# Kernel optimization log

Hardware: AMD Instinct MI355X
Metric: run time of the kernel (lower is better)

Reference implementation:

```python
import jax, jax.numpy as jnp
import numpy as np

B, L, C = 4, 4096, 2048
NH, K = 32, 16
F = C // NH  # head_dim = 64
LR = 1.0     # config.inner_net_lr
EPS = 1e-6


def setup_inputs() -> dict:
    key = jax.random.key(0)
    ks = jax.random.split(key, 8)
    s = 0.02
    return {
        "hidden_states": jax.random.normal(ks[0], (B, L, C), jnp.float32),
        "q_w": jax.random.normal(ks[1], (C, C), jnp.float32) * s,
        "k_w": jax.random.normal(ks[2], (C, C), jnp.float32) * s,
        "v_w": jax.random.normal(ks[3], (C, C), jnp.float32) * s,
        "o_w": jax.random.normal(ks[4], (C, C), jnp.float32) * s,
        "lin_w": jax.random.normal(ks[5], (NH, 1, C), jnp.float32) * s,
        "lin_b": jnp.zeros((NH, 1), jnp.float32),
        "ln_w": jnp.ones((NH, F), jnp.float32),
        "ln_b": jnp.zeros((NH, F), jnp.float32),
        "W1": jax.random.normal(ks[6], (NH, F, F), jnp.float32) * s,
        "b1": jnp.zeros((NH, 1, F), jnp.float32),
    }


def _ln(z, g, b):
    # LayerNormFunction.forward over last dim (head_dim)
    mu = z.mean(-1, keepdims=True)
    var = jnp.mean((z - mu) ** 2, axis=-1, keepdims=True)
    x_hat = (z - mu) * jax.lax.rsqrt(var + EPS)
    return g * x_hat + b


def _ln_l2_bwd(z, target, g, b):
    # decoder_ln_bwd: grad of 0.5*||LN(z) - target||^2 w.r.t. z, fused LN fwd+bwd
    mu = z.mean(-1, keepdims=True)
    var = jnp.mean((z - mu) ** 2, axis=-1, keepdims=True)
    std = jnp.sqrt(var + EPS)
    x_hat = (z - mu) / std
    gy = (g * x_hat + b - target) * g  # grad_x_hat
    return (F * gy - gy.sum(-1, keepdims=True)
            - x_hat * (gy * x_hat).sum(-1, keepdims=True)) / (F * std)


def reference(hidden_states, q_w, k_w, v_w, o_w, lin_w, lin_b, ln_w, ln_b, W1, b1):
    nc = L // K  # number of inner chunks

    def proj(w):
        x = hidden_states @ w.T                      # [B,L,C]
        x = x.reshape(B, nc, K, NH, F)
        return jnp.moveaxis(x, 3, 1)                 # [B,NH,nc,K,F]

    XC, XB, XA = proj(q_w), proj(k_w), proj(v_w)

    # per-head ilr gate: vmap(F.linear) over heads, softplus activation
    Xr = hidden_states.reshape(B, nc, K, C)
    ilr = jax.nn.softplus(jnp.einsum('bnkc,hoc->bhnko', Xr, lin_w)
                          + lin_b[None, :, None, None, :])   # [B,NH,nc,K,1]
    token_idx = 1.0 / jnp.arange(1, K + 1, dtype=jnp.float32)
    coeff = (LR * token_idx)[None, None, None, :, None] * ilr / F  # [B,NH,nc,K,1]

    gamma = ln_w[None, :, None, :]  # [1,NH,1,F]
    beta = ln_b[None, :, None, :]
    mask = jnp.tril(jnp.ones((K, K), jnp.float32))

    W1_0 = jnp.broadcast_to(W1[None], (B, NH, F, F))
    b1_0 = jnp.broadcast_to(b1[None], (B, NH, 1, F))

    def step(carry, xs):
        W1s, b1s = carry
        xa, xb, xc, co = xs                 # [B,NH,K,F], co: [B,NH,K,1]
        Z1 = xb @ W1s + b1s                 # inner-net forward
        gZ = _ln_l2_bwd(Z1, xa - xb, gamma, beta)  # grad_l_wrt_Z1
        Attn1 = (xc @ jnp.swapaxes(xb, -1, -2)) * mask      # tril(XC XB^T) [B,NH,K,K]
        b1_bar = b1s - (co * mask) @ gZ                      # [B,NH,K,F]
        Z1_bar = xc @ W1s - (co * Attn1) @ gZ + b1_bar       # dual-form output
        co_last = co[:, :, -1:, :]                           # [B,NH,1,1]
        W1_new = W1s - jnp.swapaxes(co_last * xb, -1, -2) @ gZ
        b1_new = b1_bar[:, :, -1:, :]
        xcw = xc + _ln(Z1_bar, gamma, beta)
        return (W1_new, b1_new), xcw

    xs = tuple(jnp.moveaxis(t, 2, 0) for t in (XA, XB, XC, coeff))
    _, out = jax.lax.scan(step, (W1_0, b1_0), xs)   # out: [nc,B,NH,K,F]
    out = jnp.moveaxis(out, 0, 1)                    # [B,nc,NH,K,F]
    out = jnp.swapaxes(out, 2, 3).reshape(B, L, C)   # [B,L,C]
    return out @ o_w.T
```

## Files before the change

kernel.cpp:

```cpp
#include <hip/hip_runtime.h>
#include <hip/hip_bf16.h>

#define B_ 4
#define L_ 4096
#define C_ 2048
#define NH_ 32
#define K_ 16
#define F_ 64
#define NC_ 256
#define EPS_ 1e-6f

typedef _Float16 half8 __attribute__((ext_vector_type(8)));
typedef _Float16 half4 __attribute__((ext_vector_type(4)));
typedef float f32x4 __attribute__((ext_vector_type(4)));

__device__ __forceinline__ float red16(float v) {
  int x;
  x = __builtin_amdgcn_update_dpp(0, __builtin_bit_cast(int, v), 0xB1, 0xF, 0xF, true);
  v += __builtin_bit_cast(float, x);
  x = __builtin_amdgcn_update_dpp(0, __builtin_bit_cast(int, v), 0x4E, 0xF, 0xF, true);
  v += __builtin_bit_cast(float, x);
  x = __builtin_amdgcn_update_dpp(0, __builtin_bit_cast(int, v), 0x124, 0xF, 0xF, true);
  v += __builtin_bit_cast(float, x);
  x = __builtin_amdgcn_update_dpp(0, __builtin_bit_cast(int, v), 0x128, 0xF, 0xF, true);
  v += __builtin_bit_cast(float, x);
  return v;
}

__device__ __forceinline__ void gl_lds16(const _Float16* g, _Float16* l) {
  __builtin_amdgcn_global_load_lds(
      (const __attribute__((address_space(1))) void*)g,
      (__attribute__((address_space(3))) void*)l, 16, 0, 0);
}

__global__ __launch_bounds__(256) void cast_f16(const float* __restrict__ in,
                                                _Float16* __restrict__ out, int n8) {
  int i = blockIdx.x * 256 + threadIdx.x;
  if (i >= n8) return;
  const float4* ip = (const float4*)in;
  float4 a = ip[2*i], b = ip[2*i+1];
  half8 o;
  o[0]=(_Float16)a.x; o[1]=(_Float16)a.y; o[2]=(_Float16)a.z; o[3]=(_Float16)a.w;
  o[4]=(_Float16)b.x; o[5]=(_Float16)b.y; o[6]=(_Float16)b.z; o[7]=(_Float16)b.w;
  ((half8*)out)[i] = o;
}

#define BM3 256
#define BN3 256
#define BK3 64

template<typename OT>
__global__ __launch_bounds__(512, 2) void gemm_f16_v3(
    const _Float16* __restrict__ A, const _Float16* __restrict__ Bm,
    OT* __restrict__ C0, OT* __restrict__ C1, OT* __restrict__ C2, int Kd)
{
  __shared__ __align__(16) _Float16 As[2][2][128*64];
  __shared__ __align__(16) _Float16 Bs[2][2][128*64];
  const int t = threadIdx.x;
  const int lane = t & 63;
  const int w = t >> 6;
  const int wr = w >> 2, wc = w & 3;
  const int bn = blockIdx.x, bm = blockIdx.y;
  const int ln = lane & 15, q = lane >> 4;

  const int srow = t >> 3, sc = t & 7;
  const int clg = sc ^ (2 * ((srow >> 2) & 1));

  auto stageA = [&](int kt, int h, int db) {
    const _Float16* g = A + ((long)(bm*BM3 + h*128 + srow))*Kd + (long)kt*BK3 + clg*8;
    gl_lds16(g,          &As[db][h][(size_t)srow*64 + sc*8]);
    gl_lds16(g + 64*Kd,  &As[db][h][(size_t)(64+srow)*64 + sc*8]);
  };
  auto stageB = [&](int kt, int h, int db) {
    const _Float16* g = Bm + ((long)(bn*BN3 + h*128 + srow))*Kd + (long)kt*BK3 + clg*8;
    gl_lds16(g,          &Bs[db][h][(size_t)srow*64 + sc*8]);
    gl_lds16(g + 64*Kd,  &Bs[db][h][(size_t)(64+srow)*64 + sc*8]);
  };

  f32x4 acc[8][4];
#pragma unroll
  for (int i = 0; i < 8; ++i)
#pragma unroll
    for (int j = 0; j < 4; ++j) acc[i][j] = (f32x4){0.f,0.f,0.f,0.f};

  half8 af[8][2], bf[4][2];

  stageA(0, 0, 0); stageA(0, 1, 0); stageB(0, 0, 0); stageB(0, 1, 0);

  const int NT = Kd / BK3;
  for (int kt = 0; kt < NT; ++kt) {
    const int db = kt & 1;
    const bool more = (kt + 1 < NT);
    if (more) { stageA(kt+1, 0, db^1); stageB(kt+1, 0, db^1); }
    __builtin_amdgcn_sched_barrier(0);
    if (more) asm volatile("s_waitcnt vmcnt(4)" ::: "memory");
    else      asm volatile("s_waitcnt vmcnt(0)" ::: "memory");
    __builtin_amdgcn_sched_barrier(0);
    __builtin_amdgcn_s_barrier();
    __builtin_amdgcn_sched_barrier(0);

    const _Float16* ap = &As[db][wr][0];
    const _Float16* bp = &Bs[db][wc >> 1][0];
    const int lcb = (wc & 1) * 64;

#pragma unroll
    for (int mi = 0; mi < 4; ++mi)
#pragma unroll
      for (int ks = 0; ks < 2; ++ks) {
        int lr = mi*16 + ln;
        int cp = (ks*4 + q) ^ (2*((lr>>2)&1));
        af[mi][ks] = *(const half8*)(ap + (size_t)lr*64 + cp*8);
      }
#pragma unroll
    for (int ni = 0; ni < 2; ++ni)
#pragma unroll
      for (int ks = 0; ks < 2; ++ks) {
        int lc = lcb + ni*16 + ln;
        int cp = (ks*4 + q) ^ (2*((lc>>2)&1));
        bf[ni][ks] = *(const half8*)(bp + (size_t)lc*64 + cp*8);
      }
    __builtin_amdgcn_s_setprio(1);
#pragma unroll
    for (int mi = 0; mi < 4; ++mi)
#pragma unroll
      for (int ni = 0; ni < 2; ++ni)
#pragma unroll
        for (int ks = 0; ks < 2; ++ks)
          acc[mi][ni] = __builtin_amdgcn_mfma_f32_16x16x32_f16(af[mi][ks], bf[ni][ks], acc[mi][ni], 0, 0, 0);
    __builtin_amdgcn_s_setprio(0);
    if (more) stageA(kt+1, 1, db^1);

#pragma unroll
    for (int mi = 4; mi < 8; ++mi)
#pragma unroll
      for (int ks = 0; ks < 2; ++ks) {
        int lr = mi*16 + ln;
        int cp = (ks*4 + q) ^ (2*((lr>>2)&1));
        af[mi][ks] = *(const half8*)(ap + (size_t)lr*64 + cp*8);
      }
    __builtin_amdgcn_s_setprio(1);
#pragma unroll
    for (int mi = 4; mi < 8; ++mi)
#pragma unroll
      for (int ni = 0; ni < 2; ++ni)
#pragma unroll
        for (int ks = 0; ks < 2; ++ks)
          acc[mi][ni] = __builtin_amdgcn_mfma_f32_16x16x32_f16(af[mi][ks], bf[ni][ks], acc[mi][ni], 0, 0, 0);
    __builtin_amdgcn_s_setprio(0);
    if (more) stageB(kt+1, 1, db^1);

#pragma unroll
    for (int ni = 2; ni < 4; ++ni)
#pragma unroll
      for (int ks = 0; ks < 2; ++ks) {
        int lc = lcb + ni*16 + ln;
        int cp = (ks*4 + q) ^ (2*((lc>>2)&1));
        bf[ni][ks] = *(const half8*)(bp + (size_t)lc*64 + cp*8);
      }
    __builtin_amdgcn_s_setprio(1);
#pragma unroll
    for (int mi = 4; mi < 8; ++mi)
#pragma unroll
      for (int ni = 2; ni < 4; ++ni)
#pragma unroll
        for (int ks = 0; ks < 2; ++ks)
          acc[mi][ni] = __builtin_amdgcn_mfma_f32_16x16x32_f16(af[mi][ks], bf[ni][ks], acc[mi][ni], 0, 0, 0);
    __builtin_amdgcn_s_setprio(0);

    __builtin_amdgcn_s_setprio(1);
#pragma unroll
    for (int mi = 0; mi < 4; ++mi)
#pragma unroll
      for (int ni = 2; ni < 4; ++ni)
#pragma unroll
        for (int ks = 0; ks < 2; ++ks)
          acc[mi][ni] = __builtin_amdgcn_mfma_f32_16x16x32_f16(af[mi][ks], bf[ni][ks], acc[mi][ni], 0, 0, 0);
    __builtin_amdgcn_s_setprio(0);

    __builtin_amdgcn_sched_barrier(0);
    __builtin_amdgcn_s_barrier();
    __builtin_amdgcn_sched_barrier(0);
  }

  const int reg = bn >> 3, bnl = bn & 7;
  OT* C = (reg == 0) ? C0 : ((reg == 1) ? C1 : C2);
  const int cr = q * 4;
#pragma unroll
  for (int mi = 0; mi < 8; ++mi)
#pragma unroll
    for (int ni = 0; ni < 4; ++ni)
#pragma unroll
      for (int r = 0; r < 4; ++r) {
        long row = (long)bm*BM3 + wr*128 + mi*16 + cr + r;
        long col = (long)bnl*256 + wc*64 + ni*16 + ln;
        C[row*2048L + col] = (OT)acc[mi][ni][r];
      }
}

__global__ __launch_bounds__(256) void ilr_kernel(
    const float* __restrict__ hid, const float* __restrict__ lin_w,
    const float* __restrict__ lin_b, float* __restrict__ coeff)
{
  const int t = threadIdx.x;
  const int lane = t & 63;
  const int w = t >> 6;
  const int row0 = blockIdx.x * 16 + w * 4;

  float4 hv[4][8];
#pragma unroll
  for (int r = 0; r < 4; ++r) {
    const float* hp = hid + (size_t)(row0 + r) * C_;
#pragma unroll
    for (int i = 0; i < 8; ++i) hv[r][i] = *(const float4*)(hp + i*256 + lane*4);
  }
  float res[4] = {0.f,0.f,0.f,0.f};
  for (int h = 0; h < NH_; ++h) {
    const float* wp = lin_w + (size_t)h * C_;
    float s[4] = {0.f,0.f,0.f,0.f};
#pragma unroll
    for (int i = 0; i < 8; ++i) {
      float4 wv = *(const float4*)(wp + i*256 + lane*4);
#pragma unroll
      for (int r = 0; r < 4; ++r)
        s[r] += hv[r][i].x*wv.x + hv[r][i].y*wv.y + hv[r][i].z*wv.z + hv[r][i].w*wv.w;
    }
#pragma unroll
    for (int o = 32; o > 0; o >>= 1)
#pragma unroll
      for (int r = 0; r < 4; ++r) s[r] += __shfl_xor(s[r], o, 64);
    if (lane == h) { res[0]=s[0]; res[1]=s[1]; res[2]=s[2]; res[3]=s[3]; }
  }
  if (lane < NH_) {
    float lb = lin_b[lane];
#pragma unroll
    for (int r = 0; r < 4; ++r) {
      int row = row0 + r;
      int b = row >> 12;
      int li = row & (L_ - 1);
      int k = li & (K_ - 1);
      float x = res[r] + lb;
      float sp = (x > 20.f) ? x : log1pf(expf(x));
      float v = (1.0f / (float)(k + 1)) * sp * (1.0f / (float)F_);
      coeff[((size_t)(b * NH_ + lane)) * L_ + li] = v;
    }
  }
}

struct Ck2 {
  half4 xbA[4], xsA[4];
  float co4[4], co15;
};

__device__ __forceinline__ void load_ck2(
    Ck2& c, const _Float16* Kp, const _Float16* S, const float* co,
    size_t rowbase, int hoff, size_t cobase, int n, int q, int ln)
{
#pragma unroll
  for (int kt = 0; kt < 4; ++kt) {
    size_t idx = (rowbase + ln) * C_ + hoff + 16*kt + 4*q;
    c.xbA[kt] = *(const half4*)(Kp + idx);
    c.xsA[kt] = *(const half4*)(S  + idx);
  }
#pragma unroll
  for (int r = 0; r < 4; ++r) c.co4[r] = co[cobase + (size_t)n*K_ + 4*q + r];
  c.co15 = co[cobase + (size_t)n*K_ + 15];
}

__global__ __launch_bounds__(128, 1) void scan_kernel(
    const _Float16* __restrict__ Q, const _Float16* __restrict__ Kp,
    const _Float16* __restrict__ V,
    const float* __restrict__ coeff, const float* __restrict__ W1g, const float* __restrict__ b1g,
    const float* __restrict__ ln_w, const float* __restrict__ ln_b,
    _Float16* __restrict__ OF)
{
  const int bh = blockIdx.x;
  const int b = bh >> 5, h = bh & 31;
  const int tid = threadIdx.x;
  const int lane = tid & 63;
  const bool isP = tid < 64;
  const int q = lane >> 4, ln = lane & 15;
  const int hoff = h * F_;
  const size_t cobase = (size_t)bh * L_;
  const size_t brow = (size_t)b * L_;

  __shared__ half4 gzs[4][4][64];

  half4 W1f[4][4];
#pragma unroll
  for (int kt = 0; kt < 4; ++kt)
#pragma unroll
    for (int t = 0; t < 4; ++t) {
      half4 hv;
#pragma unroll
      for (int j = 0; j < 4; ++j)
        hv[j] = (_Float16)W1g[(size_t)h*F_*F_ + (size_t)(16*kt + 4*q + j)*F_ + 16*t + ln];
      W1f[kt][t] = hv;
    }
  float b1r[4], gamt[4], bett[4];
#pragma unroll
  for (int t = 0; t < 4; ++t) {
    b1r[t]  = b1g[hoff + 16*t + ln];
    gamt[t] = ln_w[hoff + 16*t + ln];
    bett[t] = ln_b[hoff + 16*t + ln];
  }
  half4 maskA, maskI;
#pragma unroll
  for (int j = 0; j < 4; ++j) {
    maskA[j] = (_Float16)((4*q + j <= ln) ? 1.f : 0.f);
    maskI[j] = (_Float16)((4*q + j == ln) ? 1.f : 0.f);
  }
  const f32x4 zf4 = (f32x4){0.f, 0.f, 0.f, 0.f};

  const _Float16* S = isP ? V : Q;

  auto iter = [&](int i, Ck2& cur, Ck2& nxt) {
    half4 gzf[4];
    half4 xbTp[4];
    float co15p = 0.f;

    if (isP) {
      if (i < NC_) {
        co15p = cur.co15;
        if (i + 1 < NC_)
          load_ck2(nxt, Kp, S, coeff, brow + (size_t)(i+1)*K_, hoff, cobase, i+1, q, ln);
        f32x4 tgD[4];
#pragma unroll
        for (int t = 0; t < 4; ++t) {
          half4 dd = cur.xsA[t] - cur.xbA[t];
          tgD[t] = __builtin_amdgcn_mfma_f32_16x16x16f16(dd, maskI, zf4, 0, 0, 0);
          f32x4 x = __builtin_amdgcn_mfma_f32_16x16x16f16(cur.xbA[t], maskI, zf4, 0, 0, 0);
          half4 v;
#pragma unroll
          for (int r = 0; r < 4; ++r) v[r] = (_Float16)x[r];
          xbTp[t] = v;
        }
        f32x4 za[4];
#pragma unroll
        for (int t = 0; t < 4; ++t) {
          f32x4 zh = (f32x4){b1r[t], b1r[t], b1r[t], b1r[t]};
#pragma unroll
          for (int kt = 0; kt < 4; ++kt)
            zh = __builtin_amdgcn_mfma_f32_16x16x16f16(cur.xbA[kt], W1f[kt][t], zh, 0, 0, 0);
          za[t] = zh;
        }
#pragma unroll
        for (int r = 0; r < 4; ++r) {
          float zr[4], s1 = 0.f, s2 = 0.f;
#pragma unroll
          for (int t = 0; t < 4; ++t) { zr[t] = za[t][r]; s1 += zr[t]; s2 += zr[t]*zr[t]; }
          s1 = red16(s1); s2 = red16(s2);
          float mu = s1 * (1.f/F_);
          float istd = rsqrtf(s2 * (1.f/F_) - mu*mu + EPS_);
          float xh[4], gy[4], sg = 0.f, sx = 0.f;
#pragma unroll
          for (int t = 0; t < 4; ++t) {
            xh[t] = (zr[t] - mu) * istd;
            gy[t] = (gamt[t]*xh[t] + bett[t] - tgD[t][r]) * gamt[t];
            sg += gy[t]; sx += gy[t]*xh[t];
          }
          sg = red16(sg); sx = red16(sx);
          const float sc = istd * (1.f/F_);
#pragma unroll
          for (int t = 0; t < 4; ++t)
            gzf[t][r] = (_Float16)((F_*gy[t] - sg - xh[t]*sx) * sc);
        }
#pragma unroll
        for (int t = 0; t < 4; ++t) gzs[i & 3][t][lane] = gzf[t];
      }
    } else {
      if (i < NC_)
        load_ck2(nxt, Kp, S, coeff, brow + (size_t)i*K_, hoff, cobase, i, q, ln);
    }

    __syncthreads();

    if (isP) {
      if (i < NC_) {
        f32x4 cum3[4];
#pragma unroll
        for (int t = 0; t < 4; ++t)
          cum3[t] = __builtin_amdgcn_mfma_f32_16x16x16f16(maskA, gzf[t], zf4, 0, 0, 0);
#pragma unroll
        for (int t = 0; t < 4; ++t) {
          float tmp = b1r[t] - co15p * cum3[t][3];
          b1r[t] = __shfl(tmp, 48 + ln, 64);
        }
#pragma unroll
        for (int mt = 0; mt < 4; ++mt)
#pragma unroll
          for (int t = 0; t < 4; ++t) {
            f32x4 d = __builtin_amdgcn_mfma_f32_16x16x16f16(xbTp[mt], gzf[t], zf4, 0, 0, 0);
            half4 dt;
#pragma unroll
            for (int r = 0; r < 4; ++r) dt[r] = (_Float16)(co15p * d[r]);
            W1f[mt][t] = W1f[mt][t] - dt;
          }
      }
    } else {
      if (i > 0) {
        const int jc = i - 1;
        const size_t rowbase = brow + (size_t)jc * K_;
        half4 gz[4];
#pragma unroll
        for (int t = 0; t < 4; ++t) gz[t] = gzs[jc & 3][t][lane];
        f32x4 xcsD[4]; half4 xbT[4];
#pragma unroll
        for (int t = 0; t < 4; ++t) {
          xcsD[t] = __builtin_amdgcn_mfma_f32_16x16x16f16(cur.xsA[t], maskI, zf4, 0, 0, 0);
          f32x4 x = __builtin_amdgcn_mfma_f32_16x16x16f16(cur.xbA[t], maskI, zf4, 0, 0, 0);
          half4 v;
#pragma unroll
          for (int r = 0; r < 4; ++r) v[r] = (_Float16)x[r];
          xbT[t] = v;
        }
        f32x4 at0 = zf4, at1 = zf4;
        at0 = __builtin_amdgcn_mfma_f32_16x16x16f16(cur.xbA[0], cur.xsA[0], at0, 0, 0, 0);
        at0 = __builtin_amdgcn_mfma_f32_16x16x16f16(cur.xbA[1], cur.xsA[1], at0, 0, 0, 0);
        at1 = __builtin_amdgcn_mfma_f32_16x16x16f16(cur.xbA[2], cur.xsA[2], at1, 0, 0, 0);
        at1 = __builtin_amdgcn_mfma_f32_16x16x16f16(cur.xbA[3], cur.xsA[3], at1, 0, 0, 0);
        f32x4 at = at0 + at1;
        half4 atf;
#pragma unroll
        for (int r = 0; r < 4; ++r) atf[r] = (_Float16)((4*q + r <= ln) ? at[r] : 0.f);
        f32x4 cum[4], ag[4];
#pragma unroll
        for (int t = 0; t < 4; ++t) {
          cum[t] = __builtin_amdgcn_mfma_f32_16x16x16f16(maskA, gz[t], zf4, 0, 0, 0);
          ag[t]  = __builtin_amdgcn_mfma_f32_16x16x16f16(atf,   gz[t], zf4, 0, 0, 0);
        }
        float zbf[4][4];
#pragma unroll
        for (int t = 0; t < 4; ++t) {
          f32x4 zh = zf4;
#pragma unroll
          for (int kt = 0; kt < 4; ++kt)
            zh = __builtin_amdgcn_mfma_f32_16x16x16f16(cur.xsA[kt], W1f[kt][t], zh, 0, 0, 0);
#pragma unroll
          for (int r = 0; r < 4; ++r)
            zbf[t][r] = zh[r] + b1r[t] - cur.co4[r]*(ag[t][r] + cum[t][r]);
        }
#pragma unroll
        for (int r = 0; r < 4; ++r) {
          float zr[4], s1 = 0.f, s2 = 0.f;
#pragma unroll
          for (int t = 0; t < 4; ++t) { zr[t] = zbf[t][r]; s1 += zr[t]; s2 += zr[t]*zr[t]; }
          s1 = red16(s1); s2 = red16(s2);
          float mu = s1 * (1.f/F_);
          float istd = rsqrtf(s2 * (1.f/F_) - mu*mu + EPS_);
#pragma unroll
          for (int t = 0; t < 4; ++t) {
            float ov = xcsD[t][r] + gamt[t]*((zr[t] - mu)*istd) + bett[t];
            OF[(rowbase + 4*q + r) * C_ + hoff + 16*t + ln] = (_Float16)ov;
          }
        }
#pragma unroll
        for (int t = 0; t < 4; ++t) {
          float tmp = b1r[t] - cur.co15 * cum[t][3];
          b1r[t] = __shfl(tmp, 48 + ln, 64);
        }
#pragma unroll
        for (int mt = 0; mt < 4; ++mt)
#pragma unroll
          for (int t = 0; t < 4; ++t) {
            f32x4 d = __builtin_amdgcn_mfma_f32_16x16x16f16(xbT[mt], gz[t], zf4, 0, 0, 0);
            half4 dt;
#pragma unroll
            for (int r = 0; r < 4; ++r) dt[r] = (_Float16)(cur.co15 * d[r]);
            W1f[mt][t] = W1f[mt][t] - dt;
          }
      }
    }
  };

  Ck2 cka, ckb;
  if (isP) load_ck2(cka, Kp, S, coeff, brow, hoff, cobase, 0, q, ln);

  for (int i = 0; i < NC_; i += 2) {
    iter(i,     cka, ckb);
    iter(i + 1, ckb, cka);
  }
  iter(NC_, cka, ckb);
}

extern "C" void kernel_launch(void* const* d_in, const int* in_sizes, int n_in,
                              void* d_out, int out_size, void* d_ws, size_t ws_size,
                              hipStream_t stream)
{
  const float* hid   = (const float*)d_in[0];
  const float* q_w   = (const float*)d_in[1];
  const float* k_w   = (const float*)d_in[2];
  const float* v_w   = (const float*)d_in[3];
  const float* o_w   = (const float*)d_in[4];
  const float* lin_w = (const float*)d_in[5];
  const float* lin_b = (const float*)d_in[6];
  const float* ln_w  = (const float*)d_in[7];
  const float* ln_b  = (const float*)d_in[8];
  const float* W1    = (const float*)d_in[9];
  const float* b1    = (const float*)d_in[10];
  float* out = (float*)d_out;

  const size_t BLC = (size_t)B_ * L_ * C_;
  const size_t CC  = (size_t)C_ * C_;
  _Float16* HF  = (_Float16*)d_ws;
  _Float16* WF3 = HF + BLC;
  _Float16* KF  = WF3 + 3*CC;
  _Float16* VF  = KF + BLC;
  float*    CO  = (float*)(VF + BLC);
  _Float16* QF  = (_Float16*)d_out;

  const int M = B_ * L_, Kd = C_;
  dim3 ggQKV(3 * C_ / BN3, M / BM3);
  dim3 ggO(C_ / BN3, M / BM3);
  const int n8h = (int)(BLC / 8);
  const int n8w = (int)(CC / 8);

  cast_f16<<<(n8h+255)/256, 256, 0, stream>>>(hid, HF, n8h);
  cast_f16<<<(n8w+255)/256, 256, 0, stream>>>(q_w, WF3,        n8w);
  cast_f16<<<(n8w+255)/256, 256, 0, stream>>>(k_w, WF3 + CC,   n8w);
  cast_f16<<<(n8w+255)/256, 256, 0, stream>>>(v_w, WF3 + 2*CC, n8w);
  gemm_f16_v3<_Float16><<<ggQKV, 512, 0, stream>>>(HF, WF3, QF, KF, VF, Kd);
  ilr_kernel<<<M / 16, 256, 0, stream>>>(hid, lin_w, lin_b, CO);
  scan_kernel<<<B_ * NH_, 128, 0, stream>>>(QF, KF, VF, CO, W1, b1, ln_w, ln_b, HF);
  cast_f16<<<(n8w+255)/256, 256, 0, stream>>>(o_w, WF3, n8w);
  gemm_f16_v3<float><<<ggO, 512, 0, stream>>>(HF, WF3, out, out, out, Kd);
}
```

Measured before the change: 1.293 ms.

## Fold ilr gate projection into QKV GEMM as extra padded column tile

The per-head ilr linear projection moves into the fused QKV fp16 GEMM by appending lin_w as an extra 256-column tile, written to a narrow scratch buffer. A small elementwise kernel then applies bias, softplus and the token scaling. This removes the separate fp32 dot-product kernel, at the cost of computing 224 padding columns from uninitialized workspace and lowering the gate logits to fp16 precision.

New measurement: 1.300 ms. No clear change (+0.5%).

```diff
diff --git a/kernel.cpp b/kernel.cpp
--- a/kernel.cpp
+++ b/kernel.cpp
@@ -52,7 +52,8 @@
 template<typename OT>
 __global__ __launch_bounds__(512, 2) void gemm_f16_v3(
     const _Float16* __restrict__ A, const _Float16* __restrict__ Bm,
-    OT* __restrict__ C0, OT* __restrict__ C1, OT* __restrict__ C2, int Kd)
+    OT* __restrict__ C0, OT* __restrict__ C1, OT* __restrict__ C2,
+    OT* __restrict__ C3, int Kd)
 {
   __shared__ __align__(16) _Float16 As[2][2][128*64];
   __shared__ __align__(16) _Float16 Bs[2][2][128*64];
@@ -183,7 +184,8 @@
   }
 
   const int reg = bn >> 3, bnl = bn & 7;
-  OT* C = (reg == 0) ? C0 : ((reg == 1) ? C1 : C2);
+  OT* C = (reg == 0) ? C0 : ((reg == 1) ? C1 : ((reg == 2) ? C2 : C3));
+  const long rstride = (reg == 3) ? 256 : 2048;
   const int cr = q * 4;
 #pragma unroll
   for (int mi = 0; mi < 8; ++mi)
@@ -193,57 +195,22 @@
       for (int r = 0; r < 4; ++r) {
         long row = (long)bm*BM3 + wr*128 + mi*16 + cr + r;
         long col = (long)bnl*256 + wc*64 + ni*16 + ln;
-        C[row*2048L + col] = (OT)acc[mi][ni][r];
-      }
-}
-
-__global__ __launch_bounds__(256) void ilr_kernel(
-    const float* __restrict__ hid, const float* __restrict__ lin_w,
-    const float* __restrict__ lin_b, float* __restrict__ coeff)
+        C[row*rstride + col] = (OT)acc[mi][ni][r];
+      }
+}
+
+__global__ __launch_bounds__(256) void ilr_post(
+    const _Float16* __restrict__ s, const float* __restrict__ lin_b,
+    float* __restrict__ coeff)
 {
-  const int t = threadIdx.x;
-  const int lane = t & 63;
-  const int w = t >> 6;
-  const int row0 = blockIdx.x * 16 + w * 4;
-
-  float4 hv[4][8];
-#pragma unroll
-  for (int r = 0; r < 4; ++r) {
-    const float* hp = hid + (size_t)(row0 + r) * C_;
-#pragma unroll
-    for (int i = 0; i < 8; ++i) hv[r][i] = *(const float4*)(hp + i*256 + lane*4);
-  }
-  float res[4] = {0.f,0.f,0.f,0.f};
-  for (int h = 0; h < NH_; ++h) {
-    const float* wp = lin_w + (size_t)h * C_;
-    float s[4] = {0.f,0.f,0.f,0.f};
-#pragma unroll
-    for (int i = 0; i < 8; ++i) {
-      float4 wv = *(const float4*)(wp + i*256 + lane*4);
-#pragma unroll
-      for (int r = 0; r < 4; ++r)
-        s[r] += hv[r][i].x*wv.x + hv[r][i].y*wv.y + hv[r][i].z*wv.z + hv[r][i].w*wv.w;
-    }
-#pragma unroll
-    for (int o = 32; o > 0; o >>= 1)
-#pragma unroll
-      for (int r = 0; r < 4; ++r) s[r] += __shfl_xor(s[r], o, 64);
-    if (lane == h) { res[0]=s[0]; res[1]=s[1]; res[2]=s[2]; res[3]=s[3]; }
-  }
-  if (lane < NH_) {
-    float lb = lin_b[lane];
-#pragma unroll
-    for (int r = 0; r < 4; ++r) {
-      int row = row0 + r;
-      int b = row >> 12;
-      int li = row & (L_ - 1);
-      int k = li & (K_ - 1);
-      float x = res[r] + lb;
-      float sp = (x > 20.f) ? x : log1pf(expf(x));
-      float v = (1.0f / (float)(k + 1)) * sp * (1.0f / (float)F_);
-      coeff[((size_t)(b * NH_ + lane)) * L_ + li] = v;
-    }
-  }
+  int i = blockIdx.x * 256 + threadIdx.x;
+  int bh = i >> 12, li = i & (L_ - 1);
+  int b = bh >> 5, h = bh & 31;
+  long row = (long)b * L_ + li;
+  float x = (float)s[row * 256 + h] + lin_b[h];
+  float sp = (x > 20.f) ? x : log1pf(expf(x));
+  int k = li & (K_ - 1);
+  coeff[(size_t)bh * L_ + li] = sp * (1.f / (float)(k + 1)) * (1.f / (float)F_);
 }
 
 struct Ck2 {
@@ -501,26 +468,31 @@
 
   const size_t BLC = (size_t)B_ * L_ * C_;
   const size_t CC  = (size_t)C_ * C_;
-  _Float16* HF  = (_Float16*)d_ws;
-  _Float16* WF3 = HF + BLC;
-  _Float16* KF  = WF3 + 3*CC;
-  _Float16* VF  = KF + BLC;
-  float*    CO  = (float*)(VF + BLC);
-  _Float16* QF  = (_Float16*)d_out;
+  const size_t ILRW = 256 * (size_t)C_;
+  const size_t ILRO = (size_t)B_ * L_ * 256;
+  _Float16* HF   = (_Float16*)d_ws;
+  _Float16* WF3  = HF + BLC;
+  _Float16* KF   = WF3 + 3*CC + ILRW;
+  _Float16* VF   = KF + BLC;
+  _Float16* SB   = VF + BLC;
+  float*    CO   = (float*)(SB + ILRO);
+  _Float16* QF   = (_Float16*)d_out;
 
   const int M = B_ * L_, Kd = C_;
-  dim3 ggQKV(3 * C_ / BN3, M / BM3);
+  dim3 ggQKV((3 * C_ + 256) / BN3, M / BM3);
   dim3 ggO(C_ / BN3, M / BM3);
   const int n8h = (int)(BLC / 8);
   const int n8w = (int)(CC / 8);
+  const int n8l = (int)(NH_ * C_ / 8);
 
   cast_f16<<<(n8h+255)/256, 256, 0, stream>>>(hid, HF, n8h);
   cast_f16<<<(n8w+255)/256, 256, 0, stream>>>(q_w, WF3,        n8w);
   cast_f16<<<(n8w+255)/256, 256, 0, stream>>>(k_w, WF3 + CC,   n8w);
   cast_f16<<<(n8w+255)/256, 256, 0, stream>>>(v_w, WF3 + 2*CC, n8w);
-  gemm_f16_v3<_Float16><<<ggQKV, 512, 0, stream>>>(HF, WF3, QF, KF, VF, Kd);
-  ilr_kernel<<<M / 16, 256, 0, stream>>>(hid, lin_w, lin_b, CO);
+  cast_f16<<<(n8l+255)/256, 256, 0, stream>>>(lin_w, WF3 + 3*CC, n8l);
+  gemm_f16_v3<_Float16><<<ggQKV, 512, 0, stream>>>(HF, WF3, QF, KF, VF, SB, Kd);
+  ilr_post<<<(B_*NH_*L_)/256, 256, 0, stream>>>(SB, lin_b, CO);
   scan_kernel<<<B_ * NH_, 128, 0, stream>>>(QF, KF, VF, CO, W1, b1, ln_w, ln_b, HF);
   cast_f16<<<(n8w+255)/256, 256, 0, stream>>>(o_w, WF3, n8w);
-  gemm_f16_v3<float><<<ggO, 512, 0, stream>>>(HF, WF3, out, out, out, Kd);
-}
+  gemm_f16_v3<float><<<ggO, 512, 0, stream>>>(HF, WF3, out, out, out, out, Kd);
+}
```
